# Optimization experiments

Hardware: AMD Instinct MI355X
Metric: run time of the kernel (lower is better)

## Reference

```python
import jax, jax.numpy as jnp
import numpy as np

B, S, D, H, V = 32, 1024, 512, 4, 8185
DH = 3 * D // H  # 384 per-head projection; q/k/v each 128
FFN = 4 * D
LN_EPS = 1e-3  # keras LayerNormalization default epsilon


def _pos_encoding(seq_len, d_model):
    pos = np.arange(seq_len)[:, None].astype(np.float32)
    i = np.arange(d_model)[None, :].astype(np.float32)
    angles = pos / np.power(10000.0, 2.0 * (i // 2) / np.float32(d_model))
    angles[:, 0::2] = np.sin(angles[:, 0::2])
    angles[:, 1::2] = np.cos(angles[:, 1::2])
    return jnp.asarray(angles, dtype=jnp.float32)  # [S, D]


def _layernorm(x, g, b):
    mu = jnp.mean(x, axis=-1, keepdims=True)
    var = jnp.mean(jnp.square(x - mu), axis=-1, keepdims=True)
    return (x - mu) * jax.lax.rsqrt(var + LN_EPS) * g + b


def setup_inputs() -> dict:
    key = jax.random.key(0)
    ks = jax.random.split(key, 8)
    sc = 0.02
    return {
        "inputs": jax.random.randint(ks[0], (B, S), 0, V, dtype=jnp.int32),
        "emb": jax.random.normal(ks[1], (V, D), jnp.float32) * sc,
        "Wp": jax.random.normal(ks[2], (H, D, DH), jnp.float32) * sc,
        "bp": jnp.zeros((H, DH), jnp.float32),
        "Wo": jax.random.normal(ks[3], (D, D), jnp.float32) * sc,
        "bo": jnp.zeros((D,), jnp.float32),
        "ln1_g": jnp.ones((D,), jnp.float32),
        "ln1_b": jnp.zeros((D,), jnp.float32),
        "W1": jax.random.normal(ks[4], (D, FFN), jnp.float32) * sc,
        "b1": jnp.zeros((FFN,), jnp.float32),
        "W2": jax.random.normal(ks[5], (FFN, D), jnp.float32) * sc,
        "b2": jnp.zeros((D,), jnp.float32),
        "ln2_g": jnp.ones((D,), jnp.float32),
        "ln2_b": jnp.zeros((D,), jnp.float32),
        "Wh": jax.random.normal(ks[6], (D, D), jnp.float32) * sc,
        "bh": jnp.zeros((D,), jnp.float32),
        "Wf": jax.random.normal(ks[7], (D, 1), jnp.float32) * sc,
        "bf": jnp.zeros((1,), jnp.float32),
    }


def reference(inputs, emb, Wp, bp, Wo, bo, ln1_g, ln1_b, W1, b1, W2, b2,
              ln2_g, ln2_b, Wh, bh, Wf, bf):
    b, s = inputs.shape
    x = emb[inputs] + _pos_encoding(s, emb.shape[1])[None]  # [B,S,D]

    # decoder block: batched per-head projections (q|k|v packed along last axis)
    res = x
    d = jnp.einsum('bsd,hde->bhse', x, Wp) + bp[:, None, :]  # [B,H,S,3*dh]
    q, k, v = jnp.split(d, 3, axis=-1)  # each [B,H,S,dh]
    # NOTE: source scales by rsqrt(seq_len) (tf.shape(k)[1]), not head dim
    scale = jax.lax.rsqrt(jnp.float32(s))
    scores = jnp.einsum('bhse,bhte->bhst', q, k) * scale  # [B,H,S,S]
    heads = jnp.einsum('bhst,bhte->bhse', scores, v)  # linear attn (no softmax)
    concat = heads.transpose(0, 2, 1, 3).reshape(b, s, -1)  # [B,S,D]
    attn = concat @ Wo + bo
    x = _layernorm(attn + res, ln1_g, ln1_b)
    h = jax.nn.relu(x @ W1 + b1) @ W2 + b2
    x = _layernorm(h + x, ln2_g, ln2_b)

    # classification head on first token
    x0 = x[:, 0]
    hid = jax.nn.relu(x0 @ Wh + bh)
    logits = hid @ Wf + bf  # [B,1]
    return logits, jax.nn.sigmoid(logits)
```

## Files before the change

### kernel.cpp

```cpp
#include <hip/hip_runtime.h>
#include <hip/hip_bf16.h>

__global__ __launch_bounds__(256) void qr_k(
    const int* __restrict__ inp, const float* __restrict__ emb,
    const float* __restrict__ Wp, const float* __restrict__ bp,
    float* __restrict__ X0, float* __restrict__ r, float* __restrict__ alpha,
    float* __restrict__ Acc, int* __restrict__ Cnt)
{
    __shared__ float xs[512];
    __shared__ float red[256];
    __shared__ float q0s[128];
    int b = blockIdx.x, h = blockIdx.y, t = threadIdx.x;
    if (b == 0 && h == 0) {
        if (t < 32) Acc[t] = 0.f;
        else if (t < 64) Cnt[t - 32] = 0;
    }
    int tok0 = inp[b * 1024];
#pragma unroll
    for (int rep = 0; rep < 2; rep++) {
        int d = t + rep * 256;
        float v = emb[(long)tok0 * 512 + d] + ((d & 1) ? 1.0f : 0.0f);
        xs[d] = v;
        if (h == 0) X0[b * 512 + d] = v;
    }
    __syncthreads();

    int f = t & 127, dh = t >> 7;
    const float* wq = Wp + (long)h * 196608 + f;
    float acc = 0.f;
#pragma unroll 8
    for (int d = dh * 256; d < dh * 256 + 256; d++)
        acc += xs[d] * wq[(long)d * 384];
    red[t] = acc;
    __syncthreads();
    if (t < 128) q0s[t] = red[t] + red[t + 128] + bp[h * 384 + t];
    __syncthreads();
    if (t < 128) red[t] = q0s[t] * bp[h * 384 + 128 + t];
    __syncthreads();
    for (int w = 64; w >= 1; w >>= 1) {
        if (t < w) red[t] += red[t + w];
        __syncthreads();
    }
    if (t == 0) alpha[b * 4 + h] = red[0];

    const float4* q4 = (const float4*)q0s;
#pragma unroll
    for (int rep = 0; rep < 2; rep++) {
        int d = t + rep * 256;
        const float4* wr = (const float4*)(Wp + ((long)(h * 512 + d)) * 384 + 128);
        float a2 = 0.f;
#pragma unroll 8
        for (int f4 = 0; f4 < 32; f4++) {
            float4 w = wr[f4], qq = q4[f4];
            a2 += w.x * qq.x + w.y * qq.y + w.z * qq.z + w.w * qq.w;
        }
        r[((long)(b * 4 + h)) * 512 + d] = a2;
    }
}

__global__ __launch_bounds__(256) void xu_k(
    const int* __restrict__ inp, const float* __restrict__ emb,
    const float* __restrict__ r, const float* __restrict__ alpha,
    float* __restrict__ Tpp, float* __restrict__ Gp)
{
    __shared__ float xs[32 * 516];
    __shared__ float rs[4 * 520];
    __shared__ float us[128];
    __shared__ int  toks[32];
    int b = blockIdx.x, sg = blockIdx.y, t = threadIdx.x;
    int wave = t >> 6, lane = t & 63;

#pragma unroll
    for (int i = 0; i < 2; i++) {
        int idx = t + i * 256;
        int h = idx >> 7, k4 = idx & 127;
        *(float4*)&rs[h * 520 + k4 * 4] =
            *(const float4*)&r[((long)(b * 4 + h)) * 512 + k4 * 4];
    }

    float w4[4];
#pragma unroll
    for (int j = 0; j < 4; j++) {
        float expo = (float)(lane * 8 + j * 2) * (1.0f / 512.0f);
        w4[j] = exp2f(-expo * 13.287712379549449f);
    }

    float accT[4][2] = {};
    float gacc = 0.f;
    for (int it = 0; it < 2; it++) {
        int s0 = (sg * 2 + it) * 32;
        __syncthreads();
        if (t < 32) toks[t] = inp[b * 1024 + s0 + t];
        __syncthreads();

#pragma unroll
        for (int i = 0; i < 8; i++) {
            int row = wave * 8 + i;
            float s = (float)(s0 + row);
            int tok = toks[row];
            const float4* e = (const float4*)&emb[(long)tok * 512 + lane * 8];
            float4 e0 = e[0], e1 = e[1];
            float sv[4], cv[4];
#pragma unroll
            for (int j = 0; j < 4; j++) {
                float ang = s * w4[j];
                sv[j] = __sinf(ang);
                cv[j] = __cosf(ang);
            }
            *(float4*)&xs[row * 516 + lane * 8] =
                make_float4(e0.x + sv[0], e0.y + cv[0], e0.z + sv[1], e0.w + cv[1]);
            *(float4*)&xs[row * 516 + lane * 8 + 4] =
                make_float4(e1.x + sv[2], e1.y + cv[2], e1.z + sv[3], e1.w + cv[3]);
        }
        __syncthreads();

        {
            int s = t >> 3, h = (t >> 1) & 3, half = t & 1;
            const float* xrow = xs + s * 516 + half * 256;
            const float* rrow = rs + h * 520 + half * 256;
            float acc = 0.f;
#pragma unroll 8
            for (int k = 0; k < 64; k++) {
                float4 xv = *(const float4*)&xrow[k * 4];
                float4 rv = *(const float4*)&rrow[k * 4];
                acc += xv.x * rv.x + xv.y * rv.y + xv.z * rv.z + xv.w * rv.w;
            }
            acc += __shfl_xor(acc, 1);
            if (half == 0) us[s * 4 + h] = acc + alpha[b * 4 + h];
        }
        __syncthreads();

        if (t < 4) {
#pragma unroll
            for (int s = 0; s < 32; s++) gacc += us[s * 4 + t];
        }

#pragma unroll 4
        for (int s = 0; s < 32; s++) {
            float x0 = xs[s * 516 + t];
            float x1 = xs[s * 516 + 256 + t];
#pragma unroll
            for (int h = 0; h < 4; h++) {
                float uv = us[s * 4 + h];
                accT[h][0] += uv * x0;
                accT[h][1] += uv * x1;
            }
        }
    }
    long base = (long)(b * 16 + sg) * 2048;
#pragma unroll
    for (int h = 0; h < 4; h++) {
        Tpp[base + h * 512 + t] = accT[h][0];
        Tpp[base + h * 512 + 256 + t] = accT[h][1];
    }
    if (t < 4) Gp[(b * 16 + sg) * 4 + t] = gacc;
}

__global__ __launch_bounds__(256) void att1_k(
    const float* __restrict__ Tpp, const float* __restrict__ Gp,
    const float* __restrict__ Wp, const float* __restrict__ bp,
    float* __restrict__ C0)
{
    __shared__ float tps[512];
    __shared__ float red[256];
    int b = blockIdx.x, jt = blockIdx.y, t = threadIdx.x;
    int h = jt >> 1, e0 = (jt & 1) * 64;
#pragma unroll
    for (int i = 0; i < 2; i++) {
        int d = t + i * 256;
        float v = 0.f;
#pragma unroll 8
        for (int sg = 0; sg < 16; sg++)
            v += Tpp[(long)b * 32768 + sg * 2048 + h * 512 + d];
        tps[d] = v;
    }
    __syncthreads();
    int e = e0 + (t & 63), rg = t >> 6;
    const float* wv = Wp + (long)h * 196608 + 256 + e;
    float acc = 0.f;
#pragma unroll 8
    for (int d = rg * 128; d < rg * 128 + 128; d++)
        acc += tps[d] * wv[(long)d * 384];
    red[t] = acc;
    __syncthreads();
    if (t < 64) {
        float gam = 0.f;
#pragma unroll
        for (int sg = 0; sg < 16; sg++) gam += Gp[(b * 16 + sg) * 4 + h];
        float sum = red[t] + red[t + 64] + red[t + 128] + red[t + 192];
        float c = 0.03125f * (sum + gam * bp[h * 384 + 256 + e0 + t]);
        C0[b * 512 + h * 128 + e0 + t] = c;
    }
}

__global__ __launch_bounds__(256) void att2s_k(
    const float* __restrict__ C0, const float* __restrict__ Wo,
    const float* __restrict__ bo, const float* __restrict__ X0,
    float* __restrict__ A1, float* __restrict__ Stat)
{
    __shared__ float c0s[512];
    __shared__ float red[256];
    int b = blockIdx.x, jt = blockIdx.y, t = threadIdx.x;
    c0s[t] = C0[b * 512 + t];
    c0s[t + 256] = C0[b * 512 + t + 256];
    __syncthreads();
    int j = jt * 64 + (t & 63), rg = t >> 6;
    float acc = 0.f;
#pragma unroll 8
    for (int d = rg * 128; d < rg * 128 + 128; d++)
        acc += c0s[d] * Wo[(long)d * 512 + j];
    red[t] = acc;
    __syncthreads();
    if (t < 64) {
        int jj = jt * 64 + t;
        float a = red[t] + red[t + 64] + red[t + 128] + red[t + 192]
                + bo[jj] + X0[b * 512 + jj];
        A1[b * 512 + jj] = a;
        float s = a, q = a * a;
#pragma unroll
        for (int off = 32; off; off >>= 1) {
            s += __shfl_down(s, off);
            q += __shfl_down(q, off);
        }
        if (t == 0) {
            Stat[(b * 8 + jt) * 2]     = s;
            Stat[(b * 8 + jt) * 2 + 1] = q;
        }
    }
}

__global__ __launch_bounds__(256) void ffn1_k(
    const float* __restrict__ A1, const float* __restrict__ Stat,
    const float* __restrict__ g1, const float* __restrict__ b1v,
    const float* __restrict__ W1, float* __restrict__ Hp1)
{
    __shared__ float at[32][128];
    __shared__ float mrs[32][2];
    int jt = blockIdx.x, ks = blockIdx.y, t = threadIdx.x;
    if (t < 32) {
        float s = 0.f, q = 0.f;
#pragma unroll
        for (int p8 = 0; p8 < 8; p8++) {
            s += Stat[(t * 8 + p8) * 2];
            q += Stat[(t * 8 + p8) * 2 + 1];
        }
        float mean = s * (1.0f / 512.0f);
        float var = q * (1.0f / 512.0f) - mean * mean;
        mrs[t][0] = mean;
        mrs[t][1] = rsqrtf(var + 0.001f);
    }
    __syncthreads();
#pragma unroll
    for (int i = 0; i < 4; i++) {
        int idx = t + i * 256;
        int row = idx >> 5, f4 = idx & 31;
        int col = ks * 128 + f4 * 4;
        float4 a4 = *(const float4*)&A1[(long)row * 512 + col];
        float4 g4 = *(const float4*)&g1[col];
        float4 bb = *(const float4*)&b1v[col];
        float mean = mrs[row][0], rstd = mrs[row][1];
        float4 v;
        v.x = (a4.x - mean) * rstd * g4.x + bb.x;
        v.y = (a4.y - mean) * rstd * g4.y + bb.y;
        v.z = (a4.z - mean) * rstd * g4.z + bb.z;
        v.w = (a4.w - mean) * rstd * g4.w + bb.w;
        ((float4*)at)[idx] = v;
    }
    __syncthreads();
    int j = jt * 64 + (t & 63), rg = t >> 6;
    float acc[8] = {};
    const float* wp = W1 + (long)(ks * 128) * 2048 + j;
#pragma unroll 4
    for (int k = 0; k < 128; k++) {
        float wv = wp[(long)k * 2048];
#pragma unroll
        for (int rr = 0; rr < 8; rr++)
            acc[rr] += at[rg * 8 + rr][k] * wv;
    }
#pragma unroll
    for (int rr = 0; rr < 8; rr++)
        Hp1[((long)(ks * 32 + rg * 8 + rr)) * 2048 + j] = acc[rr];
}

__global__ __launch_bounds__(256) void ffn2_k(
    const float* __restrict__ Hp1, const float* __restrict__ b1,
    const float* __restrict__ W2, float* __restrict__ Hp2)
{
    __shared__ float at[32][128];
    int jt = blockIdx.x, ks = blockIdx.y, t = threadIdx.x;
#pragma unroll
    for (int i = 0; i < 4; i++) {
        int idx = t + i * 256;
        int row = idx >> 5, f4 = idx & 31;
        int col4 = ks * 32 + f4;
        float4 v = ((const float4*)b1)[col4];
#pragma unroll
        for (int p = 0; p < 4; p++) {
            float4 pv = ((const float4*)Hp1)[(long)p * 16384 + (long)row * 512 + col4];
            v.x += pv.x; v.y += pv.y; v.z += pv.z; v.w += pv.w;
        }
        v.x = fmaxf(v.x, 0.f); v.y = fmaxf(v.y, 0.f);
        v.z = fmaxf(v.z, 0.f); v.w = fmaxf(v.w, 0.f);
        ((float4*)at)[idx] = v;
    }
    __syncthreads();
    int j = jt * 64 + (t & 63), rg = t >> 6;
    float acc[8] = {};
    const float* wp = W2 + (long)(ks * 128) * 512 + j;
#pragma unroll 4
    for (int k = 0; k < 128; k++) {
        float wv = wp[(long)k * 512];
#pragma unroll
        for (int rr = 0; rr < 8; rr++)
            acc[rr] += at[rg * 8 + rr][k] * wv;
    }
#pragma unroll
    for (int rr = 0; rr < 8; rr++)
        Hp2[((long)(ks * 32 + rg * 8 + rr)) * 512 + j] = acc[rr];
}

__global__ __launch_bounds__(256) void headp3_k(
    const float* __restrict__ Hp2, const float* __restrict__ b2,
    const float* __restrict__ A1, const float* __restrict__ Stat,
    const float* __restrict__ g1v, const float* __restrict__ b1v,
    const float* __restrict__ g2v, const float* __restrict__ b2v,
    const float* __restrict__ Wh, const float* __restrict__ bh,
    const float* __restrict__ Wf, const float* __restrict__ bf,
    float* __restrict__ Acc, int* __restrict__ Cnt, float* __restrict__ out)
{
    __shared__ float xs[512];
    __shared__ float red[256];
    __shared__ float sd[8];
    __shared__ float mr[2];
    int b = blockIdx.x, jt = blockIdx.y, t = threadIdx.x;
    if (t == 0) {
        float s = 0.f, q = 0.f;
#pragma unroll
        for (int p8 = 0; p8 < 8; p8++) {
            s += Stat[(b * 8 + p8) * 2];
            q += Stat[(b * 8 + p8) * 2 + 1];
        }
        float mean = s * (1.0f / 512.0f);
        mr[0] = mean;
        mr[1] = rsqrtf(q * (1.0f / 512.0f) - mean * mean + 0.001f);
    }
    __syncthreads();
    float mean1 = mr[0], rstd1 = mr[1];
    float a[2];
#pragma unroll
    for (int rep = 0; rep < 2; rep++) {
        int j = t + rep * 256;
        float y1 = (A1[b * 512 + j] - mean1) * rstd1 * g1v[j] + b1v[j];
        float v = b2[j] + y1;
#pragma unroll
        for (int ks = 0; ks < 16; ks++)
            v += Hp2[((long)(ks * 32 + b)) * 512 + j];
        a[rep] = v;
    }
    float s = a[0] + a[1];
#pragma unroll
    for (int off = 32; off; off >>= 1) s += __shfl_down(s, off);
    if ((t & 63) == 0) sd[t >> 6] = s;
    __syncthreads();
    float mean = (sd[0] + sd[1] + sd[2] + sd[3]) * (1.0f / 512.0f);
    float d0 = a[0] - mean, d1 = a[1] - mean;
    float v2 = d0 * d0 + d1 * d1;
#pragma unroll
    for (int off = 32; off; off >>= 1) v2 += __shfl_down(v2, off);
    if ((t & 63) == 0) sd[4 + (t >> 6)] = v2;
    __syncthreads();
    float var = (sd[4] + sd[5] + sd[6] + sd[7]) * (1.0f / 512.0f);
    float rstd = rsqrtf(var + 0.001f);
    xs[t] = d0 * rstd * g2v[t] + b2v[t];
    xs[t + 256] = d1 * rstd * g2v[t + 256] + b2v[t + 256];
    __syncthreads();

    int j = jt * 64 + (t & 63), rg = t >> 6;
    const float* w = Wh + j;
    float acc = 0.f;
#pragma unroll 8
    for (int d = rg * 128; d < rg * 128 + 128; d++)
        acc += xs[d] * w[(long)d * 512];
    red[t] = acc;
    __syncthreads();
    if (t < 64) {
        int jj = jt * 64 + t;
        float hid = red[t] + red[t + 64] + red[t + 128] + red[t + 192] + bh[jj];
        hid = fmaxf(hid, 0.f);
        float p = hid * Wf[jj];
#pragma unroll
        for (int off = 32; off; off >>= 1) p += __shfl_down(p, off);
        if (t == 0) {
            atomicAdd(&Acc[b], p);
            __threadfence();
            int old = atomicAdd(&Cnt[b], 1);
            if (old == 7) {
                float tot = atomicAdd(&Acc[b], 0.0f);
                float logit = tot + bf[0];
                out[b] = logit;
                out[32 + b] = 1.f / (1.f + expf(-logit));
            }
        }
    }
}

extern "C" void kernel_launch(void* const* d_in, const int* in_sizes, int n_in,
                              void* d_out, int out_size, void* d_ws, size_t ws_size,
                              hipStream_t stream)
{
    const int*   inputs = (const int*)  d_in[0];
    const float* emb    = (const float*)d_in[1];
    const float* Wp     = (const float*)d_in[2];
    const float* bp     = (const float*)d_in[3];
    const float* Wo     = (const float*)d_in[4];
    const float* bo     = (const float*)d_in[5];
    const float* ln1_g  = (const float*)d_in[6];
    const float* ln1_b  = (const float*)d_in[7];
    const float* W1     = (const float*)d_in[8];
    const float* b1     = (const float*)d_in[9];
    const float* W2     = (const float*)d_in[10];
    const float* b2     = (const float*)d_in[11];
    const float* ln2_g  = (const float*)d_in[12];
    const float* ln2_b  = (const float*)d_in[13];
    const float* Wh     = (const float*)d_in[14];
    const float* bh     = (const float*)d_in[15];
    const float* Wf     = (const float*)d_in[16];
    const float* bf     = (const float*)d_in[17];
    float* out = (float*)d_out;

    char* p = (char*)d_ws;
    float* X0    = (float*)p;  p += 65536;
    float* r     = (float*)p;  p += 262144;
    float* alpha = (float*)p;  p += 1024;
    float* Gp    = (float*)p;  p += 8192;
    float* Tpp   = (float*)p;  p += 4194304;
    float* C0    = (float*)p;  p += 65536;
    float* A1    = (float*)p;  p += 65536;
    float* Stat  = (float*)p;  p += 2048;
    float* Acc   = (float*)p;  p += 512;
    int*   Cnt   = (int*)p;    p += 512;
    float* Hp1   = (float*)p;  p += 1048576;
    float* Hp2   = (float*)p;  p += 1048576;

    qr_k<<<dim3(32, 4), 256, 0, stream>>>(inputs, emb, Wp, bp, X0, r, alpha,
                                          Acc, Cnt);
    xu_k<<<dim3(32, 16), 256, 0, stream>>>(inputs, emb, r, alpha, Tpp, Gp);
    att1_k<<<dim3(32, 8), 256, 0, stream>>>(Tpp, Gp, Wp, bp, C0);
    att2s_k<<<dim3(32, 8), 256, 0, stream>>>(C0, Wo, bo, X0, A1, Stat);
    ffn1_k<<<dim3(32, 4), 256, 0, stream>>>(A1, Stat, ln1_g, ln1_b, W1, Hp1);
    ffn2_k<<<dim3(8, 16), 256, 0, stream>>>(Hp1, b1, W2, Hp2);
    headp3_k<<<dim3(32, 8), 256, 0, stream>>>(Hp2, b2, A1, Stat,
                                              ln1_g, ln1_b, ln2_g, ln2_b,
                                              Wh, bh, Wf, bf, Acc, Cnt, out);
}
```

Baseline: 197.2 us.

## Fuse dependent stages into two kernels with global atomic counters

Merges att1 and att2s into one launch, and ffn1, ffn2 and the head into another. Consumer blocks spin on global atomic counters until producer blocks signal completion, replacing kernel boundaries as the synchronisation point. This removes launch gaps between small kernels. It relies on producer blocks being scheduled before or alongside waiting blocks, which risks deadlock or wasted CU slots while blocks spin.

```diff
diff --git a/kernel.cpp b/kernel.cpp
--- a/kernel.cpp
+++ b/kernel.cpp
@@ -5,16 +5,13 @@
     const int* __restrict__ inp, const float* __restrict__ emb,
     const float* __restrict__ Wp, const float* __restrict__ bp,
     float* __restrict__ X0, float* __restrict__ r, float* __restrict__ alpha,
-    float* __restrict__ Acc, int* __restrict__ Cnt)
+    int* __restrict__ zbase)
 {
     __shared__ float xs[512];
     __shared__ float red[256];
     __shared__ float q0s[128];
     int b = blockIdx.x, h = blockIdx.y, t = threadIdx.x;
-    if (b == 0 && h == 0) {
-        if (t < 32) Acc[t] = 0.f;
-        else if (t < 64) Cnt[t - 32] = 0;
-    }
+    if (b == 0 && h == 0 && t < 128) zbase[t] = 0;
     int tok0 = inp[b * 1024];
 #pragma unroll
     for (int rep = 0; rep < 2; rep++) {
@@ -156,249 +153,270 @@
     if (t < 4) Gp[(b * 16 + sg) * 4 + t] = gacc;
 }
 
-__global__ __launch_bounds__(256) void att1_k(
+__global__ __launch_bounds__(256) void attf_k(
     const float* __restrict__ Tpp, const float* __restrict__ Gp,
     const float* __restrict__ Wp, const float* __restrict__ bp,
-    float* __restrict__ C0)
+    const float* __restrict__ Wo, const float* __restrict__ bo,
+    const float* __restrict__ X0, float* __restrict__ C0,
+    float* __restrict__ A1, float* __restrict__ Stat, int* __restrict__ cntA)
 {
     __shared__ float tps[512];
     __shared__ float red[256];
-    int b = blockIdx.x, jt = blockIdx.y, t = threadIdx.x;
-    int h = jt >> 1, e0 = (jt & 1) * 64;
-#pragma unroll
-    for (int i = 0; i < 2; i++) {
-        int d = t + i * 256;
-        float v = 0.f;
-#pragma unroll 8
-        for (int sg = 0; sg < 16; sg++)
-            v += Tpp[(long)b * 32768 + sg * 2048 + h * 512 + d];
-        tps[d] = v;
-    }
-    __syncthreads();
-    int e = e0 + (t & 63), rg = t >> 6;
-    const float* wv = Wp + (long)h * 196608 + 256 + e;
-    float acc = 0.f;
-#pragma unroll 8
-    for (int d = rg * 128; d < rg * 128 + 128; d++)
-        acc += tps[d] * wv[(long)d * 384];
-    red[t] = acc;
-    __syncthreads();
-    if (t < 64) {
-        float gam = 0.f;
-#pragma unroll
-        for (int sg = 0; sg < 16; sg++) gam += Gp[(b * 16 + sg) * 4 + h];
-        float sum = red[t] + red[t + 64] + red[t + 128] + red[t + 192];
-        float c = 0.03125f * (sum + gam * bp[h * 384 + 256 + e0 + t]);
-        C0[b * 512 + h * 128 + e0 + t] = c;
+    int b = blockIdx.x, role = blockIdx.y, t = threadIdx.x;
+
+    if (role < 8) {
+        int jt = role;
+        int h = jt >> 1, e0 = (jt & 1) * 64;
+#pragma unroll
+        for (int i = 0; i < 2; i++) {
+            int d = t + i * 256;
+            float v = 0.f;
+#pragma unroll 8
+            for (int sg = 0; sg < 16; sg++)
+                v += Tpp[(long)b * 32768 + sg * 2048 + h * 512 + d];
+            tps[d] = v;
+        }
+        __syncthreads();
+        int e = e0 + (t & 63), rg = t >> 6;
+        const float* wv = Wp + (long)h * 196608 + 256 + e;
+        float acc = 0.f;
+#pragma unroll 8
+        for (int d = rg * 128; d < rg * 128 + 128; d++)
+            acc += tps[d] * wv[(long)d * 384];
+        red[t] = acc;
+        __syncthreads();
+        if (t < 64) {
+            float gam = 0.f;
+#pragma unroll
+            for (int sg = 0; sg < 16; sg++) gam += Gp[(b * 16 + sg) * 4 + h];
+            float sum = red[t] + red[t + 64] + red[t + 128] + red[t + 192];
+            float c = 0.03125f * (sum + gam * bp[h * 384 + 256 + e0 + t]);
+            C0[b * 512 + h * 128 + e0 + t] = c;
+        }
+        __syncthreads();
+        if (t == 0) {
+            __threadfence();
+            atomicAdd(&cntA[b], 1);
+        }
+    } else {
+        int jt = role - 8;
+        if (t == 0) {
+            while (atomicAdd(&cntA[b], 0) < 8) __builtin_amdgcn_s_sleep(2);
+            __threadfence();
+        }
+        __syncthreads();
+        float* c0s = tps;
+        c0s[t] = C0[b * 512 + t];
+        c0s[t + 256] = C0[b * 512 + t + 256];
+        __syncthreads();
+        int j = jt * 64 + (t & 63), rg = t >> 6;
+        float acc = 0.f;
+#pragma unroll 8
+        for (int d = rg * 128; d < rg * 128 + 128; d++)
+            acc += c0s[d] * Wo[(long)d * 512 + j];
+        red[t] = acc;
+        __syncthreads();
+        if (t < 64) {
+            int jj = jt * 64 + t;
+            float a = red[t] + red[t + 64] + red[t + 128] + red[t + 192]
+                    + bo[jj] + X0[b * 512 + jj];
+            A1[b * 512 + jj] = a;
+            float s = a, q = a * a;
+#pragma unroll
+            for (int off = 32; off; off >>= 1) {
+                s += __shfl_down(s, off);
+                q += __shfl_down(q, off);
+            }
+            if (t == 0) {
+                Stat[(b * 8 + jt) * 2]     = s;
+                Stat[(b * 8 + jt) * 2 + 1] = q;
+            }
+        }
     }
 }
 
-__global__ __launch_bounds__(256) void att2s_k(
-    const float* __restrict__ C0, const float* __restrict__ Wo,
-    const float* __restrict__ bo, const float* __restrict__ X0,
-    float* __restrict__ A1, float* __restrict__ Stat)
-{
-    __shared__ float c0s[512];
-    __shared__ float red[256];
-    int b = blockIdx.x, jt = blockIdx.y, t = threadIdx.x;
-    c0s[t] = C0[b * 512 + t];
-    c0s[t + 256] = C0[b * 512 + t + 256];
-    __syncthreads();
-    int j = jt * 64 + (t & 63), rg = t >> 6;
-    float acc = 0.f;
-#pragma unroll 8
-    for (int d = rg * 128; d < rg * 128 + 128; d++)
-        acc += c0s[d] * Wo[(long)d * 512 + j];
-    red[t] = acc;
-    __syncthreads();
-    if (t < 64) {
-        int jj = jt * 64 + t;
-        float a = red[t] + red[t + 64] + red[t + 128] + red[t + 192]
-                + bo[jj] + X0[b * 512 + jj];
-        A1[b * 512 + jj] = a;
-        float s = a, q = a * a;
-#pragma unroll
-        for (int off = 32; off; off >>= 1) {
-            s += __shfl_down(s, off);
-            q += __shfl_down(q, off);
-        }
-        if (t == 0) {
-            Stat[(b * 8 + jt) * 2]     = s;
-            Stat[(b * 8 + jt) * 2 + 1] = q;
-        }
-    }
-}
-
-__global__ __launch_bounds__(256) void ffn1_k(
+__global__ __launch_bounds__(256) void fh_k(
     const float* __restrict__ A1, const float* __restrict__ Stat,
-    const float* __restrict__ g1, const float* __restrict__ b1v,
-    const float* __restrict__ W1, float* __restrict__ Hp1)
+    const float* __restrict__ g1v, const float* __restrict__ b1v,
+    const float* __restrict__ W1, const float* __restrict__ b1,
+    const float* __restrict__ W2, const float* __restrict__ b2,
+    const float* __restrict__ g2v, const float* __restrict__ b2v,
+    const float* __restrict__ Wh, const float* __restrict__ bh,
+    const float* __restrict__ Wf, const float* __restrict__ bf,
+    float* __restrict__ Hp1, float* __restrict__ Hp2,
+    int* __restrict__ cntCD, float* __restrict__ Acc, int* __restrict__ Cnt,
+    float* __restrict__ out)
 {
     __shared__ float at[32][128];
     __shared__ float mrs[32][2];
-    int jt = blockIdx.x, ks = blockIdx.y, t = threadIdx.x;
-    if (t < 32) {
-        float s = 0.f, q = 0.f;
-#pragma unroll
-        for (int p8 = 0; p8 < 8; p8++) {
-            s += Stat[(t * 8 + p8) * 2];
-            q += Stat[(t * 8 + p8) * 2 + 1];
-        }
-        float mean = s * (1.0f / 512.0f);
-        float var = q * (1.0f / 512.0f) - mean * mean;
-        mrs[t][0] = mean;
-        mrs[t][1] = rsqrtf(var + 0.001f);
-    }
-    __syncthreads();
-#pragma unroll
-    for (int i = 0; i < 4; i++) {
-        int idx = t + i * 256;
-        int row = idx >> 5, f4 = idx & 31;
-        int col = ks * 128 + f4 * 4;
-        float4 a4 = *(const float4*)&A1[(long)row * 512 + col];
-        float4 g4 = *(const float4*)&g1[col];
-        float4 bb = *(const float4*)&b1v[col];
-        float mean = mrs[row][0], rstd = mrs[row][1];
-        float4 v;
-        v.x = (a4.x - mean) * rstd * g4.x + bb.x;
-        v.y = (a4.y - mean) * rstd * g4.y + bb.y;
-        v.z = (a4.z - mean) * rstd * g4.z + bb.z;
-        v.w = (a4.w - mean) * rstd * g4.w + bb.w;
-        ((float4*)at)[idx] = v;
-    }
-    __syncthreads();
-    int j = jt * 64 + (t & 63), rg = t >> 6;
-    float acc[8] = {};
-    const float* wp = W1 + (long)(ks * 128) * 2048 + j;
-#pragma unroll 4
-    for (int k = 0; k < 128; k++) {
-        float wv = wp[(long)k * 2048];
-#pragma unroll
-        for (int rr = 0; rr < 8; rr++)
-            acc[rr] += at[rg * 8 + rr][k] * wv;
-    }
-#pragma unroll
-    for (int rr = 0; rr < 8; rr++)
-        Hp1[((long)(ks * 32 + rg * 8 + rr)) * 2048 + j] = acc[rr];
-}
-
-__global__ __launch_bounds__(256) void ffn2_k(
-    const float* __restrict__ Hp1, const float* __restrict__ b1,
-    const float* __restrict__ W2, float* __restrict__ Hp2)
-{
-    __shared__ float at[32][128];
-    int jt = blockIdx.x, ks = blockIdx.y, t = threadIdx.x;
-#pragma unroll
-    for (int i = 0; i < 4; i++) {
-        int idx = t + i * 256;
-        int row = idx >> 5, f4 = idx & 31;
-        int col4 = ks * 32 + f4;
-        float4 v = ((const float4*)b1)[col4];
-#pragma unroll
-        for (int p = 0; p < 4; p++) {
-            float4 pv = ((const float4*)Hp1)[(long)p * 16384 + (long)row * 512 + col4];
-            v.x += pv.x; v.y += pv.y; v.z += pv.z; v.w += pv.w;
-        }
-        v.x = fmaxf(v.x, 0.f); v.y = fmaxf(v.y, 0.f);
-        v.z = fmaxf(v.z, 0.f); v.w = fmaxf(v.w, 0.f);
-        ((float4*)at)[idx] = v;
-    }
-    __syncthreads();
-    int j = jt * 64 + (t & 63), rg = t >> 6;
-    float acc[8] = {};
-    const float* wp = W2 + (long)(ks * 128) * 512 + j;
-#pragma unroll 4
-    for (int k = 0; k < 128; k++) {
-        float wv = wp[(long)k * 512];
-#pragma unroll
-        for (int rr = 0; rr < 8; rr++)
-            acc[rr] += at[rg * 8 + rr][k] * wv;
-    }
-#pragma unroll
-    for (int rr = 0; rr < 8; rr++)
-        Hp2[((long)(ks * 32 + rg * 8 + rr)) * 512 + j] = acc[rr];
-}
-
-__global__ __launch_bounds__(256) void headp3_k(
-    const float* __restrict__ Hp2, const float* __restrict__ b2,
-    const float* __restrict__ A1, const float* __restrict__ Stat,
-    const float* __restrict__ g1v, const float* __restrict__ b1v,
-    const float* __restrict__ g2v, const float* __restrict__ b2v,
-    const float* __restrict__ Wh, const float* __restrict__ bh,
-    const float* __restrict__ Wf, const float* __restrict__ bf,
-    float* __restrict__ Acc, int* __restrict__ Cnt, float* __restrict__ out)
-{
     __shared__ float xs[512];
     __shared__ float red[256];
     __shared__ float sd[8];
     __shared__ float mr[2];
-    int b = blockIdx.x, jt = blockIdx.y, t = threadIdx.x;
-    if (t == 0) {
-        float s = 0.f, q = 0.f;
-#pragma unroll
-        for (int p8 = 0; p8 < 8; p8++) {
-            s += Stat[(b * 8 + p8) * 2];
-            q += Stat[(b * 8 + p8) * 2 + 1];
-        }
-        float mean = s * (1.0f / 512.0f);
-        mr[0] = mean;
-        mr[1] = rsqrtf(q * (1.0f / 512.0f) - mean * mean + 0.001f);
-    }
-    __syncthreads();
-    float mean1 = mr[0], rstd1 = mr[1];
-    float a[2];
-#pragma unroll
-    for (int rep = 0; rep < 2; rep++) {
-        int j = t + rep * 256;
-        float y1 = (A1[b * 512 + j] - mean1) * rstd1 * g1v[j] + b1v[j];
-        float v = b2[j] + y1;
-#pragma unroll
-        for (int ks = 0; ks < 16; ks++)
-            v += Hp2[((long)(ks * 32 + b)) * 512 + j];
-        a[rep] = v;
-    }
-    float s = a[0] + a[1];
-#pragma unroll
-    for (int off = 32; off; off >>= 1) s += __shfl_down(s, off);
-    if ((t & 63) == 0) sd[t >> 6] = s;
-    __syncthreads();
-    float mean = (sd[0] + sd[1] + sd[2] + sd[3]) * (1.0f / 512.0f);
-    float d0 = a[0] - mean, d1 = a[1] - mean;
-    float v2 = d0 * d0 + d1 * d1;
-#pragma unroll
-    for (int off = 32; off; off >>= 1) v2 += __shfl_down(v2, off);
-    if ((t & 63) == 0) sd[4 + (t >> 6)] = v2;
-    __syncthreads();
-    float var = (sd[4] + sd[5] + sd[6] + sd[7]) * (1.0f / 512.0f);
-    float rstd = rsqrtf(var + 0.001f);
-    xs[t] = d0 * rstd * g2v[t] + b2v[t];
-    xs[t + 256] = d1 * rstd * g2v[t + 256] + b2v[t + 256];
-    __syncthreads();
-
-    int j = jt * 64 + (t & 63), rg = t >> 6;
-    const float* w = Wh + j;
-    float acc = 0.f;
-#pragma unroll 8
-    for (int d = rg * 128; d < rg * 128 + 128; d++)
-        acc += xs[d] * w[(long)d * 512];
-    red[t] = acc;
-    __syncthreads();
-    if (t < 64) {
-        int jj = jt * 64 + t;
-        float hid = red[t] + red[t + 64] + red[t + 128] + red[t + 192] + bh[jj];
-        hid = fmaxf(hid, 0.f);
-        float p = hid * Wf[jj];
-#pragma unroll
-        for (int off = 32; off; off >>= 1) p += __shfl_down(p, off);
-        if (t == 0) {
-            atomicAdd(&Acc[b], p);
-            __threadfence();
-            int old = atomicAdd(&Cnt[b], 1);
-            if (old == 7) {
-                float tot = atomicAdd(&Acc[b], 0.0f);
-                float logit = tot + bf[0];
-                out[b] = logit;
-                out[32 + b] = 1.f / (1.f + expf(-logit));
+    int z = blockIdx.x, t = threadIdx.x;
+
+    if (z < 128) {
+        int jt = z & 31, ks = z >> 5;
+        if (t < 32) {
+            float s = 0.f, q = 0.f;
+#pragma unroll
+            for (int p8 = 0; p8 < 8; p8++) {
+                s += Stat[(t * 8 + p8) * 2];
+                q += Stat[(t * 8 + p8) * 2 + 1];
+            }
+            float mean = s * (1.0f / 512.0f);
+            float var = q * (1.0f / 512.0f) - mean * mean;
+            mrs[t][0] = mean;
+            mrs[t][1] = rsqrtf(var + 0.001f);
+        }
+        __syncthreads();
+#pragma unroll
+        for (int i = 0; i < 4; i++) {
+            int idx = t + i * 256;
+            int row = idx >> 5, f4 = idx & 31;
+            int col = ks * 128 + f4 * 4;
+            float4 a4 = *(const float4*)&A1[(long)row * 512 + col];
+            float4 g4 = *(const float4*)&g1v[col];
+            float4 bb = *(const float4*)&b1v[col];
+            float mean = mrs[row][0], rstd = mrs[row][1];
+            float4 v;
+            v.x = (a4.x - mean) * rstd * g4.x + bb.x;
+            v.y = (a4.y - mean) * rstd * g4.y + bb.y;
+            v.z = (a4.z - mean) * rstd * g4.z + bb.z;
+            v.w = (a4.w - mean) * rstd * g4.w + bb.w;
+            ((float4*)at)[idx] = v;
+        }
+        __syncthreads();
+        int j = jt * 64 + (t & 63), rg = t >> 6;
+        float acc[8] = {};
+        const float* wp = W1 + (long)(ks * 128) * 2048 + j;
+#pragma unroll 4
+        for (int k = 0; k < 128; k++) {
+            float wv = wp[(long)k * 2048];
+#pragma unroll
+            for (int rr = 0; rr < 8; rr++)
+                acc[rr] += at[rg * 8 + rr][k] * wv;
+        }
+#pragma unroll
+        for (int rr = 0; rr < 8; rr++)
+            Hp1[((long)(ks * 32 + rg * 8 + rr)) * 2048 + j] = acc[rr];
+        __syncthreads();
+        if (t == 0) {
+            __threadfence();
+            atomicAdd(&cntCD[0], 1);
+        }
+    } else if (z < 256) {
+        int i2 = z - 128, jt = i2 & 7, ks = i2 >> 3;
+        if (t == 0) {
+            while (atomicAdd(&cntCD[0], 0) < 128) __builtin_amdgcn_s_sleep(8);
+            __threadfence();
+        }
+        __syncthreads();
+#pragma unroll
+        for (int i = 0; i < 4; i++) {
+            int idx = t + i * 256;
+            int row = idx >> 5, f4 = idx & 31;
+            int col4 = ks * 32 + f4;
+            float4 v = ((const float4*)b1)[col4];
+#pragma unroll
+            for (int p = 0; p < 4; p++) {
+                float4 pv = ((const float4*)Hp1)[(long)p * 16384 + (long)row * 512 + col4];
+                v.x += pv.x; v.y += pv.y; v.z += pv.z; v.w += pv.w;
+            }
+            v.x = fmaxf(v.x, 0.f); v.y = fmaxf(v.y, 0.f);
+            v.z = fmaxf(v.z, 0.f); v.w = fmaxf(v.w, 0.f);
+            ((float4*)at)[idx] = v;
+        }
+        __syncthreads();
+        int j = jt * 64 + (t & 63), rg = t >> 6;
+        float acc[8] = {};
+        const float* wp = W2 + (long)(ks * 128) * 512 + j;
+#pragma unroll 4
+        for (int k = 0; k < 128; k++) {
+            float wv = wp[(long)k * 512];
+#pragma unroll
+            for (int rr = 0; rr < 8; rr++)
+                acc[rr] += at[rg * 8 + rr][k] * wv;
+        }
+#pragma unroll
+        for (int rr = 0; rr < 8; rr++)
+            Hp2[((long)(ks * 32 + rg * 8 + rr)) * 512 + j] = acc[rr];
+        __syncthreads();
+        if (t == 0) {
+            __threadfence();
+            atomicAdd(&cntCD[1], 1);
+        }
+    } else {
+        int i2 = z - 256, b = i2 >> 3, jt = i2 & 7;
+        if (t == 0) {
+            while (atomicAdd(&cntCD[1], 0) < 128) __builtin_amdgcn_s_sleep(8);
+            __threadfence();
+            float s = 0.f, q = 0.f;
+#pragma unroll
+            for (int p8 = 0; p8 < 8; p8++) {
+                s += Stat[(b * 8 + p8) * 2];
+                q += Stat[(b * 8 + p8) * 2 + 1];
+            }
+            float mean = s * (1.0f / 512.0f);
+            mr[0] = mean;
+            mr[1] = rsqrtf(q * (1.0f / 512.0f) - mean * mean + 0.001f);
+        }
+        __syncthreads();
+        float mean1 = mr[0], rstd1 = mr[1];
+        float a[2];
+#pragma unroll
+        for (int rep = 0; rep < 2; rep++) {
+            int j = t + rep * 256;
+            float y1 = (A1[b * 512 + j] - mean1) * rstd1 * g1v[j] + b1v[j];
+            float v = b2[j] + y1;
+#pragma unroll
+            for (int ks = 0; ks < 16; ks++)
+                v += Hp2[((long)(ks * 32 + b)) * 512 + j];
+            a[rep] = v;
+        }
+        float s = a[0] + a[1];
+#pragma unroll
+        for (int off = 32; off; off >>= 1) s += __shfl_down(s, off);
+        if ((t & 63) == 0) sd[t >> 6] = s;
+        __syncthreads();
+        float mean = (sd[0] + sd[1] + sd[2] + sd[3]) * (1.0f / 512.0f);
+        float d0 = a[0] - mean, d1 = a[1] - mean;
+        float v2 = d0 * d0 + d1 * d1;
+#pragma unroll
+        for (int off = 32; off; off >>= 1) v2 += __shfl_down(v2, off);
+        if ((t & 63) == 0) sd[4 + (t >> 6)] = v2;
+        __syncthreads();
+        float var = (sd[4] + sd[5] + sd[6] + sd[7]) * (1.0f / 512.0f);
+        float rstd = rsqrtf(var + 0.001f);
+        xs[t] = d0 * rstd * g2v[t] + b2v[t];
+        xs[t + 256] = d1 * rstd * g2v[t + 256] + b2v[t + 256];
+        __syncthreads();
+
+        int j = jt * 64 + (t & 63), rg = t >> 6;
+        const float* w = Wh + j;
+        float acc = 0.f;
+#pragma unroll 8
+        for (int d = rg * 128; d < rg * 128 + 128; d++)
+            acc += xs[d] * w[(long)d * 512];
+        red[t] = acc;
+        __syncthreads();
+        if (t < 64) {
+            int jj = jt * 64 + t;
+            float hid = red[t] + red[t + 64] + red[t + 128] + red[t + 192] + bh[jj];
+            hid = fmaxf(hid, 0.f);
+            float p = hid * Wf[jj];
+#pragma unroll
+            for (int off = 32; off; off >>= 1) p += __shfl_down(p, off);
+            if (t == 0) {
+                atomicAdd(&Acc[b], p);
+                __threadfence();
+                int old = atomicAdd(&Cnt[b], 1);
+                if (old == 7) {
+                    float tot = atomicAdd(&Acc[b], 0.0f);
+                    float logit = tot + bf[0];
+                    out[b] = logit;
+                    out[32 + b] = 1.f / (1.f + expf(-logit));
+                }
             }
         }
     }
@@ -437,19 +455,20 @@
     float* C0    = (float*)p;  p += 65536;
     float* A1    = (float*)p;  p += 65536;
     float* Stat  = (float*)p;  p += 2048;
-    float* Acc   = (float*)p;  p += 512;
-    int*   Cnt   = (int*)p;    p += 512;
+    int*   zbase = (int*)p;    p += 512;
+    float* Acc   = (float*)zbase;
+    int*   Cnt   = zbase + 32;
+    int*   cntA  = zbase + 64;
+    int*   cntCD = zbase + 96;
     float* Hp1   = (float*)p;  p += 1048576;
     float* Hp2   = (float*)p;  p += 1048576;
 
     qr_k<<<dim3(32, 4), 256, 0, stream>>>(inputs, emb, Wp, bp, X0, r, alpha,
-                                          Acc, Cnt);
+                                          zbase);
     xu_k<<<dim3(32, 16), 256, 0, stream>>>(inputs, emb, r, alpha, Tpp, Gp);
-    att1_k<<<dim3(32, 8), 256, 0, stream>>>(Tpp, Gp, Wp, bp, C0);
-    att2s_k<<<dim3(32, 8), 256, 0, stream>>>(C0, Wo, bo, X0, A1, Stat);
-    ffn1_k<<<dim3(32, 4), 256, 0, stream>>>(A1, Stat, ln1_g, ln1_b, W1, Hp1);
-    ffn2_k<<<dim3(8, 16), 256, 0, stream>>>(Hp1, b1, W2, Hp2);
-    headp3_k<<<dim3(32, 8), 256, 0, stream>>>(Hp2, b2, A1, Stat,
-                                              ln1_g, ln1_b, ln2_g, ln2_b,
-                                              Wh, bh, Wf, bf, Acc, Cnt, out);
+    attf_k<<<dim3(32, 16), 256, 0, stream>>>(Tpp, Gp, Wp, bp, Wo, bo, X0,
+                                             C0, A1, Stat, cntA);
+    fh_k<<<512, 256, 0, stream>>>(A1, Stat, ln1_g, ln1_b, W1, b1, W2, b2,
+                                  ln2_g, ln2_b, Wh, bh, Wf, bf,
+                                  Hp1, Hp2, cntCD, Acc, Cnt, out);
 }
```

Result: slower. 241.9 us (+22.7%).
